# Kernel optimization log

Measured on AMD Instinct MI355X. Metric: run time of the kernel, lower is better.

The kernel has to match this reference:

```python
import jax, jax.numpy as jnp
import numpy as np

EMB, HID, NCH, CHK = 512, 1024, 16, 64   # hid_sz=1024, chunk_sz=64 -> 16 chunks
K, V = 5, 32000                           # n_mixtures, vocab
B, T = 8, 129
GATE = 4 * HID + 2 * NCH                  # i,f,o,g plus 2 master gates over chunks


def setup_inputs() -> dict:
    key = jax.random.key(0)
    ks = jax.random.split(key, 12)
    w = lambda k, shape: jax.random.normal(k, shape, jnp.float32) * 0.05
    return {
        "ys_token": jax.random.randint(ks[0], (B, T), 0, V),
        "emb": w(ks[1], (V, EMB)).at[0].set(0.0),  # padding_idx=0 row zeroed
        "Wx0": w(ks[2], (EMB, GATE)), "Wh0": w(ks[3], (HID, GATE)), "b0": jnp.zeros((GATE,), jnp.float32),
        "Wx1": w(ks[4], (HID, GATE)), "Wh1": w(ks[5], (HID, GATE)), "b1": jnp.zeros((GATE,), jnp.float32),
        "Wx2": w(ks[6], (HID, GATE)), "Wh2": w(ks[7], (HID, GATE)), "b2": jnp.zeros((GATE,), jnp.float32),
        "Wp": w(ks[8], (HID, K)), "bp": jnp.zeros((K,), jnp.float32),
        "Wl": w(ks[9], (HID, K * HID)), "bl": jnp.zeros((K * HID,), jnp.float32),
        "Wo": w(ks[10], (HID, V)), "bo": jnp.zeros((V,), jnp.float32),
    }


def _onlstm_cell(x, h, c, Wx, Wh, b):
    """One ON-LSTM step. Returns (h', c', master_forget_cumax)."""
    proj = x @ Wx + h @ Wh + b
    gates, masters = proj[:, : 4 * HID], proj[:, 4 * HID :]
    i, f, o, g = jnp.split(gates, 4, axis=-1)
    i, f, o = jax.nn.sigmoid(i), jax.nn.sigmoid(f), jax.nn.sigmoid(o)
    g = jnp.tanh(g)
    mf, mi = jnp.split(masters, 2, axis=-1)            # (B, NCH) each
    tf = jnp.cumsum(jax.nn.softmax(mf, -1), -1)        # master forget: cumax
    ti = 1.0 - jnp.cumsum(jax.nn.softmax(mi, -1), -1)  # master input: 1 - cumax
    tfe = jnp.repeat(tf, CHK, axis=-1)                 # expand chunks to HID
    tie = jnp.repeat(ti, CHK, axis=-1)
    w_ = tfe * tie
    c2 = (f * w_ + (tfe - w_)) * c + (i * w_ + (tie - w_)) * g
    h2 = o * jnp.tanh(c2)
    return h2, c2, tf


def reference(ys_token, emb, Wx0, Wh0, b0, Wx1, Wh1, b1, Wx2, Wh2, b2, Wp, bp, Wl, bl, Wo, bo):
    ys_in = ys_token[:, :-1]
    x = emb[ys_in]                                     # (B, T-1, EMB)
    z = jnp.zeros((B, HID), jnp.float32)

    def step(carry, xt):
        h0, c0, h1, c1, h2, c2 = carry
        h0, c0, _ = _onlstm_cell(xt, h0, c0, Wx0, Wh0, b0)
        h1, c1, tf1 = _onlstm_cell(h0, h1, c1, Wx1, Wh1, b1)  # s_layer = 1
        h2, c2, _ = _onlstm_cell(h1, h2, c2, Wx2, Wh2, b2)
        df = NCH - jnp.sum(tf1, -1)                    # expected split depth (B,)
        return (h0, c0, h1, c1, h2, c2), (h2, tf1, df)

    _, (outs, cf, df) = jax.lax.scan(step, (z, z, z, z, z, z), jnp.swapaxes(x, 0, 1))
    h = jnp.swapaxes(outs, 0, 1)                       # (B, L, HID)
    cf = jnp.swapaxes(cf, 0, 1)                        # (B, L, NCH)
    df = jnp.swapaxes(df, 0, 1)                        # (B, L)

    # Mixture-of-Softmaxes predictor
    log_prior = jax.nn.log_softmax(h @ Wp + bp, -1)    # (B, L, K)
    lat = jnp.tanh(h @ Wl + bl).reshape(B, T - 1, K, HID)
    mix = jax.nn.log_softmax(jnp.einsum("blkh,hv->blkv", lat, Wo) + bo, -1)
    logp = jax.nn.logsumexp(log_prior[..., None] + mix, axis=2)  # (B, L, V) log-probs

    gold = ys_token[:, 1:]
    mask = (gold != 0).astype(jnp.float32)
    nll = -jnp.take_along_axis(logp, gold[..., None], -1)[..., 0]
    per_seq = jnp.sum(nll * mask, 1) / (jnp.sum(mask, 1) + 1e-13)
    loss = jnp.mean(per_seq)
    pred = jnp.argmax(logp, -1)
    return loss, df, cf, pred
```

## Files before the change

kernel.cpp:

```cpp
#include <hip/hip_runtime.h>
#include <stdint.h>
#include <stddef.h>

#define TT   128
#define GATE 4128
#define VOC  32000
#define NWG  256

typedef float  f32x4 __attribute__((ext_vector_type(4)));
typedef short  bf16x8 __attribute__((ext_vector_type(8)));
typedef unsigned short u16x4 __attribute__((ext_vector_type(4)));

__device__ __forceinline__ float bf2f(ushort u){
  union { uint32_t i; float f; } c; c.i = ((uint32_t)u) << 16; return c.f;
}
__device__ __forceinline__ ushort f2bf(float x){
  uint32_t u = __builtin_bit_cast(uint32_t, x);
  uint32_t r = (u + 0x7fffu + ((u >> 16) & 1u)) >> 16;
  return (ushort)r;
}

__global__ void embed_kernel(const int* __restrict__ ys, const float* __restrict__ emb,
                             float* __restrict__ x){
  int r = blockIdx.x;
  int t = r >> 3, b = r & 7;
  int tok = ys[b*129 + t];
  f32x4 v = *(const f32x4*)&emb[(size_t)tok*512 + threadIdx.x*4];
  *(f32x4*)&x[(size_t)r*512 + threadIdx.x*4] = v;
}

__global__ void whT_kernel(const float* __restrict__ Wh, float* __restrict__ WhT){
  __shared__ float tile[32][33];
  int g0 = blockIdx.x*32, k0 = blockIdx.y*32;
  int tx = threadIdx.x, ty = threadIdx.y;
  for (int i = ty; i < 32; i += 8)
    tile[i][tx] = Wh[(size_t)(k0+i)*GATE + g0 + tx];
  __syncthreads();
  for (int i = ty; i < 32; i += 8)
    WhT[(size_t)(g0+i)*1024 + k0 + tx] = tile[tx][i];
}

__global__ void whmT_kernel(const float* __restrict__ Wh, float* __restrict__ WhmT){
  int idx = blockIdx.x*256 + threadIdx.x;
  int k = idx >> 5, c = idx & 31;
  WhmT[idx] = Wh[(size_t)k*GATE + 4096 + c];
}

template<int MODE>
__global__ __launch_bounds__(256) void gemm_f32_kernel(
    const float* __restrict__ X, const float* __restrict__ W, const float* __restrict__ bias,
    float* __restrict__ O1, int Kdim, int N)
{
  __shared__ float At[2][8][132];
  __shared__ float Bs[2][8][132];
  int tid = threadIdx.x;
  int n0 = blockIdx.x*128, r0 = blockIdx.y*128;
  int tx = tid & 15, ty = tid >> 4;
  int am = tid >> 1, akq = tid & 1;
  int bk = tid >> 5, bnc = tid & 31;
  float acc[8][8];
  #pragma unroll
  for (int i=0;i<8;i++)
    #pragma unroll
    for (int j=0;j<8;j++) acc[i][j]=0.f;
  {
    f32x4 av = *(const f32x4*)&X[(size_t)(r0+am)*Kdim + akq*4];
    At[0][akq*4+0][am]=av.x; At[0][akq*4+1][am]=av.y; At[0][akq*4+2][am]=av.z; At[0][akq*4+3][am]=av.w;
    int nb = n0 + bnc*4;
    f32x4 bv = {0.f,0.f,0.f,0.f};
    if (nb + 3 < N) bv = *(const f32x4*)&W[(size_t)bk*N + nb];
    *(f32x4*)&Bs[0][bk][bnc*4] = bv;
  }
  __syncthreads();
  int nk = Kdim >> 3;
  for (int ksb = 0; ksb < nk; ksb++){
    int cb = ksb & 1;
    if (ksb + 1 < nk){
      int k0 = (ksb+1)*8, bs = cb^1;
      f32x4 av = *(const f32x4*)&X[(size_t)(r0+am)*Kdim + k0 + akq*4];
      At[bs][akq*4+0][am]=av.x; At[bs][akq*4+1][am]=av.y; At[bs][akq*4+2][am]=av.z; At[bs][akq*4+3][am]=av.w;
      int nb = n0 + bnc*4;
      f32x4 bv = {0.f,0.f,0.f,0.f};
      if (nb + 3 < N) bv = *(const f32x4*)&W[(size_t)(k0+bk)*N + nb];
      *(f32x4*)&Bs[bs][bk][bnc*4] = bv;
    }
    #pragma unroll
    for (int k = 0; k < 8; k++){
      float a[8], b[8];
      *(f32x4*)&a[0] = *(const f32x4*)&At[cb][k][ty*8];
      *(f32x4*)&a[4] = *(const f32x4*)&At[cb][k][ty*8+4];
      *(f32x4*)&b[0] = *(const f32x4*)&Bs[cb][k][tx*8];
      *(f32x4*)&b[4] = *(const f32x4*)&Bs[cb][k][tx*8+4];
      #pragma unroll
      for (int i=0;i<8;i++)
        #pragma unroll
        for (int j=0;j<8;j++) acc[i][j] = fmaf(a[i], b[j], acc[i][j]);
    }
    __syncthreads();
  }
  #pragma unroll
  for (int i=0;i<8;i++){
    int r = r0 + ty*8 + i;
    #pragma unroll
    for (int j=0;j<8;j+=4){
      int n = n0 + tx*8 + j;
      if (n + 3 < N){
        f32x4 v;
        v.x = acc[i][j+0] + bias[n+0];
        v.y = acc[i][j+1] + bias[n+1];
        v.z = acc[i][j+2] + bias[n+2];
        v.w = acc[i][j+3] + bias[n+3];
        if (MODE == 1){
          v.x = tanhf(v.x); v.y = tanhf(v.y); v.z = tanhf(v.z); v.w = tanhf(v.w);
        }
        *(f32x4*)&O1[(size_t)r*N + n] = v;
      }
    }
  }
}

__global__ __launch_bounds__(256) void latsplit_kernel(const float* __restrict__ latf,
                                                       ushort* __restrict__ hi, ushort* __restrict__ lo){
  int i = (blockIdx.x*256 + threadIdx.x)*4;
  f32x4 v = *(const f32x4*)&latf[i];
  u16x4 h, l;
  #pragma unroll
  for (int j = 0; j < 4; j++){
    ushort hb = f2bf(v[j]);
    h[j] = hb;
    l[j] = f2bf(v[j] - bf2f(hb));
  }
  *(u16x4*)&hi[i] = h;
  *(u16x4*)&lo[i] = l;
}

__device__ __forceinline__ void gbar(int* flags, int* gen, int ep, int wg, int tid){
  if (wg == 0){
    if (tid == 0){
      __threadfence();
      __hip_atomic_store(&flags[0], ep, __ATOMIC_RELAXED, __HIP_MEMORY_SCOPE_AGENT);
    }
    if (tid < NWG){
      while (__hip_atomic_load(&flags[tid*16], __ATOMIC_RELAXED, __HIP_MEMORY_SCOPE_AGENT) < ep)
        __builtin_amdgcn_s_sleep(1);
    }
    __syncthreads();
    if (tid == 0){
      __threadfence();
      __hip_atomic_store(gen, ep, __ATOMIC_RELAXED, __HIP_MEMORY_SCOPE_AGENT);
      __threadfence();
    }
  } else {
    if (tid == 0){
      __threadfence();
      __hip_atomic_store(&flags[wg*16], ep, __ATOMIC_RELAXED, __HIP_MEMORY_SCOPE_AGENT);
      while (__hip_atomic_load(gen, __ATOMIC_RELAXED, __HIP_MEMORY_SCOPE_AGENT) < ep)
        __builtin_amdgcn_s_sleep(2);
      __threadfence();
    }
  }
}

__global__ __launch_bounds__(512) void scan_kernel(
    const float* __restrict__ A,
    const float* __restrict__ WhT,
    const float* __restrict__ WhmT,
    float* __restrict__ hbuf,
    float* __restrict__ H,
    float* __restrict__ cf_out, float* __restrict__ df_out,
    int* bar_flags, int* bar_gen, int* mflags, float* tfti)
{
  __shared__ __align__(16) float wls[1024*20];
  __shared__ __align__(16) float hls[1024*12];
  __shared__ __align__(16) float gpw[2][2][32][36];
  __shared__ float projg[8][16];
  __shared__ float cst[8][4];
  __shared__ float mpart[8][8][4];
  __shared__ float projmb[32];

  int tid = threadIdx.x, wg = blockIdx.x;
  int e0 = wg*4, chunk = wg >> 4;

  #pragma unroll
  for (int c = 0; c < 16; c++){
    int gcol = (c>>2)*1024 + e0 + (c&3);
    const float* src = WhT + (size_t)gcol*1024;
    for (int k = tid; k < 1024; k += 512)
      wls[k*20 + c] = src[k];
  }
  if (tid < 32) cst[tid & 7][tid >> 3] = 0.f;
  __syncthreads();

  int cq = tid >> 8;
  int bh = (tid >> 7) & 1;
  int kp = tid & 127;
  bool isM = (wg < 8);
  int mcg = tid & 7, mkp = tid >> 3;

  for (int t = 0; t < TT; t++){
    int rb = (t+1) & 1, wb = t & 1;
    float Ag = 0.f;
    if (tid < 128){
      int c = tid >> 3, b = tid & 7;
      Ag = A[(size_t)(t*8+b)*GATE + (c>>2)*1024 + e0 + (c&3)];
    }
    float Am = 0.f;
    if (isM && tid < 32) Am = A[(size_t)(t*8+wg)*GATE + 4096 + tid];

    {
      const f32x4* hb4 = (const f32x4*)&hbuf[rb*8192];
      #pragma unroll
      for (int s2 = 0; s2 < 4; s2++){
        int i4 = s2*512 + tid;
        f32x4 v = hb4[i4];
        int k = i4 >> 1, h2 = i4 & 1;
        *(f32x4*)&hls[k*12 + h2*4] = v;
      }
    }
    __syncthreads();

    if (isM){
      float macc[4] = {0.f,0.f,0.f,0.f};
      #pragma unroll
      for (int j = 0; j < 16; j++){
        int k = j*64 + mkp;
        f32x4 wm = *(const f32x4*)&WhmT[k*32 + mcg*4];
        float hv = hls[k*12 + wg];
        macc[0] += wm.x*hv; macc[1] += wm.y*hv; macc[2] += wm.z*hv; macc[3] += wm.w*hv;
      }
      #pragma unroll
      for (int off = 8; off < 64; off <<= 1){
        macc[0] += __shfl_xor(macc[0], off);
        macc[1] += __shfl_xor(macc[1], off);
        macc[2] += __shfl_xor(macc[2], off);
        macc[3] += __shfl_xor(macc[3], off);
      }
      if ((tid & 63) < 8){
        int wv = tid >> 6;
        mpart[wv][mcg][0] = macc[0]; mpart[wv][mcg][1] = macc[1];
        mpart[wv][mcg][2] = macc[2]; mpart[wv][mcg][3] = macc[3];
      }
      __syncthreads();
      if (tid < 32){
        float s = Am;
        #pragma unroll
        for (int wv = 0; wv < 8; wv++) s += mpart[wv][tid>>2][tid&3];
        projmb[tid] = s;
      }
      __syncthreads();
      if (tid == 0){
        float mx1 = -1e30f, mx2 = -1e30f;
        #pragma unroll
        for (int j = 0; j < 16; j++){
          mx1 = fmaxf(mx1, projmb[j]);
          mx2 = fmaxf(mx2, projmb[16+j]);
        }
        float e1[16], e2[16], s1 = 0.f, s2 = 0.f;
        #pragma unroll
        for (int j = 0; j < 16; j++){
          e1[j] = expf(projmb[j]    - mx1); s1 += e1[j];
          e2[j] = expf(projmb[16+j] - mx2); s2 += e2[j];
        }
        float r1 = 0.f, r2 = 0.f, tsum = 0.f;
        #pragma unroll
        for (int j = 0; j < 16; j++){
          r1 += e1[j]/s1; tfti[wg*16 + j] = r1; tsum += r1;
          r2 += e2[j]/s2; tfti[128 + wg*16 + j] = 1.f - r2;
        }
        if (cf_out != nullptr){
          #pragma unroll
          for (int j = 0; j < 16; j++) cf_out[(wg*TT + t)*16 + j] = tfti[wg*16 + j];
          df_out[wg*TT + t] = 16.0f - tsum;
        }
        __threadfence();
        __hip_atomic_store(&mflags[wg*16], t+1, __ATOMIC_RELAXED, __HIP_MEMORY_SCOPE_AGENT);
      }
    }

    float acc[8][4];
    #pragma unroll
    for (int c = 0; c < 8; c++)
      #pragma unroll
      for (int b2 = 0; b2 < 4; b2++) acc[c][b2] = 0.f;
    #pragma unroll
    for (int j = 0; j < 8; j++){
      int k = j*128 + kp;
      float wa[8], hb[4];
      *(f32x4*)&wa[0] = *(const f32x4*)&wls[k*20 + cq*8];
      *(f32x4*)&wa[4] = *(const f32x4*)&wls[k*20 + cq*8 + 4];
      *(f32x4*)&hb[0] = *(const f32x4*)&hls[k*12 + bh*4];
      #pragma unroll
      for (int c = 0; c < 8; c++)
        #pragma unroll
        for (int b2 = 0; b2 < 4; b2++)
          acc[c][b2] = fmaf(wa[c], hb[b2], acc[c][b2]);
    }
    #pragma unroll
    for (int c = 0; c < 8; c++)
      #pragma unroll
      for (int b2 = 0; b2 < 4; b2++){
        float v = acc[c][b2];
        v += __shfl_xor(v, 1);
        v += __shfl_xor(v, 2);
        acc[c][b2] = v;
      }
    if ((kp & 3) == 0){
      int kg = kp >> 2;
      #pragma unroll
      for (int c = 0; c < 8; c++){
        f32x4 v4 = { acc[c][0], acc[c][1], acc[c][2], acc[c][3] };
        *(f32x4*)&gpw[cq][bh][kg][c*4] = v4;
      }
    }
    __syncthreads();
    if (tid < 128){
      int c = tid >> 3, b = tid & 7;
      float s = Ag;
      #pragma unroll
      for (int g = 0; g < 32; g++) s += gpw[c>>3][b>>2][g][(c&7)*4 + (b&3)];
      projg[b][c] = s;
    }
    if (tid < 8){
      while (__hip_atomic_load(&mflags[tid*16], __ATOMIC_RELAXED, __HIP_MEMORY_SCOPE_AGENT) < t+1)
        __builtin_amdgcn_s_sleep(1);
    }
    __syncthreads();
    if (tid < 32){
      int b = tid & 7, e = tid >> 3;
      float gi = projg[b][e], gf = projg[b][4+e], go = projg[b][8+e], gg = projg[b][12+e];
      float iv = 1.f/(1.f+expf(-gi)), fv = 1.f/(1.f+expf(-gf)), ov = 1.f/(1.f+expf(-go));
      float gv = tanhf(gg);
      float tf = __hip_atomic_load(&tfti[b*16 + chunk],       __ATOMIC_RELAXED, __HIP_MEMORY_SCOPE_AGENT);
      float ti = __hip_atomic_load(&tfti[128 + b*16 + chunk], __ATOMIC_RELAXED, __HIP_MEMORY_SCOPE_AGENT);
      float w  = tf*ti;
      float c2 = (fv*w + (tf - w))*cst[b][e] + (iv*w + (ti - w))*gv;
      cst[b][e] = c2;
      float h2 = ov * tanhf(c2);
      hbuf[wb*8192 + (e0+e)*8 + b] = h2;
      H[(size_t)(t*8+b)*1024 + e0 + e] = h2;
    }
    __syncthreads();
    gbar(bar_flags, bar_gen, t+1, wg, tid);
    __syncthreads();
  }
}

__device__ __forceinline__ void stageA_lds(const ushort* gsrc, char* ldsbase, int row0, int k0, int tid){
  int lane = tid & 63, wv = tid >> 6;
  #pragma unroll
  for (int s = 0; s < 2; s++){
    int p = wv*1024 + s*4096 + lane*16;
    int row = p >> 6;
    int kg  = (p >> 4) & 3;
    int kgs = kg ^ ((row >> 1) & 3);
    const ushort* ga = gsrc + (size_t)(row0 + row)*1024 + k0 + kgs*8;
    __builtin_amdgcn_global_load_lds(
        (const __attribute__((address_space(1))) void*)ga,
        (__attribute__((address_space(3))) void*)(ldsbase + wv*1024 + s*4096),
        16, 0, 0);
  }
}
__device__ __forceinline__ void stageB(const float* __restrict__ Wo, int n0, int k0, int tid,
                                       char* bhi, char* blo){
  int kp = tid & 15, g = tid >> 4;
  const float* src = Wo + (size_t)(k0 + 2*kp)*VOC + n0 + g*8;
  f32x4 v00 = *(const f32x4*)(src);
  f32x4 v01 = *(const f32x4*)(src + 4);
  f32x4 v10 = *(const f32x4*)(src + VOC);
  f32x4 v11 = *(const f32x4*)(src + VOC + 4);
  int kg = kp >> 2, sub = kp & 3;
  #pragma unroll
  for (int j = 0; j < 8; j++){
    float x0 = (j < 4) ? v00[j] : v01[j-4];
    float x1 = (j < 4) ? v10[j] : v11[j-4];
    ushort h0 = f2bf(x0), h1 = f2bf(x1);
    ushort l0 = f2bf(x0 - bf2f(h0)), l1 = f2bf(x1 - bf2f(h1));
    int n = g*8 + j;
    int byte = n*64 + ((kg ^ ((n >> 1) & 3)) << 4) + sub*4;
    *(uint32_t*)(bhi + byte) = (uint32_t)h0 | ((uint32_t)h1 << 16);
    *(uint32_t*)(blo + byte) = (uint32_t)l0 | ((uint32_t)l1 << 16);
  }
}
__device__ __forceinline__ bf16x8 rdfrag(const char* base, int row, int kg){
  int byte = row*64 + ((kg ^ ((row >> 1) & 3)) << 4);
  return *(const bf16x8*)(base + byte);
}

__global__ __launch_bounds__(256) void wo_gemm_kernel(
    const ushort* __restrict__ Ahi, const ushort* __restrict__ Alo,
    const float* __restrict__ Wo, const float* __restrict__ bo,
    float* __restrict__ S, float* __restrict__ partials, int rowbase)
{
  __shared__ __align__(16) char smem[66560];
  __shared__ float bo_s[128];
  __shared__ float redm[128][2], reds[128][2];
  int tid = threadIdx.x;
  int nt = blockIdx.x, mt = blockIdx.y;
  int n0 = nt*128, row0loc = mt*128, row0 = rowbase + row0loc;
  if (tid < 128) bo_s[tid] = bo[n0 + tid];
  f32x4 acc[4][4] = {};

  stageA_lds(Ahi, smem + 0,    row0, 0, tid);
  stageA_lds(Alo, smem + 8192, row0, 0, tid);
  stageB(Wo, n0, 0, tid, smem + 16384, smem + 24576);
  __syncthreads();

  int lane = tid & 63, wv = tid >> 6;
  int wr = wv >> 1, wc = wv & 1;
  int rl = lane & 15, kgl = lane >> 4;
  for (int ks = 0; ks < 32; ks++){
    char* cb = smem + (ks & 1)*32768;
    if (ks + 1 < 32){
      char* nb2 = smem + ((ks+1) & 1)*32768;
      stageA_lds(Ahi, nb2,        row0, (ks+1)*32, tid);
      stageA_lds(Alo, nb2 + 8192, row0, (ks+1)*32, tid);
      stageB(Wo, n0, (ks+1)*32, tid, nb2 + 16384, nb2 + 24576);
    }
    bf16x8 ah[4], al[4], bh[4], bl2[4];
    #pragma unroll
    for (int m = 0; m < 4; m++){
      int row = wr*64 + m*16 + rl;
      ah[m] = rdfrag(cb,        row, kgl);
      al[m] = rdfrag(cb + 8192, row, kgl);
    }
    #pragma unroll
    for (int n = 0; n < 4; n++){
      int rw = wc*64 + n*16 + rl;
      bh[n]  = rdfrag(cb + 16384, rw, kgl);
      bl2[n] = rdfrag(cb + 24576, rw, kgl);
    }
    #pragma unroll
    for (int m = 0; m < 4; m++)
      #pragma unroll
      for (int n = 0; n < 4; n++){
        acc[m][n] = __builtin_amdgcn_mfma_f32_16x16x32_bf16(ah[m], bh[n],  acc[m][n], 0,0,0);
        acc[m][n] = __builtin_amdgcn_mfma_f32_16x16x32_bf16(ah[m], bl2[n], acc[m][n], 0,0,0);
        acc[m][n] = __builtin_amdgcn_mfma_f32_16x16x32_bf16(al[m], bh[n],  acc[m][n], 0,0,0);
      }
    __syncthreads();
  }

  float* st = (float*)smem;
  #pragma unroll
  for (int m = 0; m < 4; m++){
    int rb = wr*64 + m*16 + (lane >> 4)*4;
    #pragma unroll
    for (int n = 0; n < 4; n++){
      int col = wc*64 + n*16 + rl;
      #pragma unroll
      for (int j = 0; j < 4; j++)
        st[(rb + j)*130 + col] = acc[m][n][j];
    }
  }
  __syncthreads();
  int row = tid >> 1, half = tid & 1;
  float lmax = -1e30f;
  for (int jc = 0; jc < 64; jc += 4){
    f32x4 v;
    #pragma unroll
    for (int j = 0; j < 4; j++){
      float x = st[row*130 + half*64 + jc + j] + bo_s[half*64 + jc + j];
      st[row*130 + half*64 + jc + j] = x;
      v[j] = x;
      lmax = fmaxf(lmax, x);
    }
    *(f32x4*)&S[(size_t)(row0loc + row)*VOC + n0 + half*64 + jc] = v;
  }
  redm[row][half] = lmax;
  __syncthreads();
  float rm = fmaxf(redm[row][0], redm[row][1]);
  float lsum = 0.f;
  for (int jc = 0; jc < 64; jc++)
    lsum += expf(st[row*130 + half*64 + jc] - rm);
  reds[row][half] = lsum;
  __syncthreads();
  if (half == 0){
    float2 pr; pr.x = rm; pr.y = reds[row][0] + reds[row][1];
    *(float2*)&partials[((size_t)(row0loc + row)*250 + nt)*2] = pr;
  }
}

__global__ void zfin_kernel(const float* __restrict__ partials, double* __restrict__ Zc, int CH){
  int rl = blockIdx.x*256 + threadIdx.x;
  if (rl >= CH) return;
  float m = -1e30f;
  for (int t2 = 0; t2 < 250; t2++) m = fmaxf(m, partials[((size_t)rl*250 + t2)*2]);
  double s = 0.0;
  for (int t2 = 0; t2 < 250; t2++){
    float pm = partials[((size_t)rl*250 + t2)*2];
    float se = partials[((size_t)rl*250 + t2)*2 + 1];
    s += exp((double)pm - (double)m)*(double)se;
  }
  Zc[rl] = (double)m + log(s);
}

__device__ __forceinline__ float cand_q(const float* __restrict__ srow, int v,
                                        float l0, float l1, float l2, float l3, float l4){
  float t0 = l0 + srow[v];
  float t1 = l1 + srow[VOC   + v];
  float t2 = l2 + srow[2*VOC + v];
  float t3 = l3 + srow[3*VOC + v];
  float t4 = l4 + srow[4*VOC + v];
  float m = fmaxf(fmaxf(fmaxf(t0,t1),fmaxf(t2,t3)),t4);
  return m + logf(expf(t0-m)+expf(t1-m)+expf(t2-m)+expf(t3-m)+expf(t4-m));
}
__global__ __launch_bounds__(256) void cand_kernel(
    const float* __restrict__ S, const double* __restrict__ lp, const double* __restrict__ Z,
    int* __restrict__ cand, int rbase)
{
  int g = blockIdx.x; int r = rbase + g; int tid = threadIdx.x;
  __shared__ float lpk[5];
  __shared__ float rq[256]; __shared__ int rv[256];
  __shared__ int cnt; __shared__ int list[64];
  if (tid < 5) lpk[tid] = (float)(lp[r*5 + tid] - Z[r*5 + tid]);
  if (tid == 0) cnt = 0;
  __syncthreads();
  float l0 = lpk[0], l1 = lpk[1], l2 = lpk[2], l3 = lpk[3], l4 = lpk[4];
  const float* srow = S + (size_t)(g*5)*VOC;
  float bq = -1e30f; int bv = 0;
  for (int v = tid; v < VOC; v += 256){
    float q = cand_q(srow, v, l0,l1,l2,l3,l4);
    if (q > bq){ bq = q; bv = v; }
  }
  rq[tid] = bq; rv[tid] = bv; __syncthreads();
  for (int s = 128; s > 0; s >>= 1){
    if (tid < s){
      if (rq[tid+s] > rq[tid] || (rq[tid+s] == rq[tid] && rv[tid+s] < rv[tid])){
        rq[tid] = rq[tid+s]; rv[tid] = rv[tid+s];
      }
    }
    __syncthreads();
  }
  float M = rq[0]; int argv = rv[0];
  for (int v = tid; v < VOC; v += 256){
    float q = cand_q(srow, v, l0,l1,l2,l3,l4);
    if (q >= M - 0.02f && v != argv){
      int ix = atomicAdd(&cnt, 1);
      if (ix < 63) list[ix] = v;
    }
  }
  __syncthreads();
  int nc = cnt < 63 ? cnt : 63;
  if (tid == 0){ cand[r*66] = nc + 1; cand[r*66 + 1] = argv; }
  if (tid < nc) cand[r*66 + 2 + tid] = list[tid];
}

__global__ __launch_bounds__(256) void refine_kernel(
    const float* __restrict__ lat, const float* __restrict__ Wo, const float* __restrict__ bo,
    const double* __restrict__ lp, const double* __restrict__ Z,
    const int* __restrict__ cand, const int* __restrict__ ys,
    float* __restrict__ nll, float* __restrict__ pred_out)
{
  int r = blockIdx.x, tid = threadIdx.x;
  int b = r & 7, l = r >> 3;
  int nc = cand[r*66];
  if (nc < 0) nc = 0;
  if (nc > 64) nc = 64;
  __shared__ double dred[5][4];
  __shared__ double bestval; __shared__ int bestv;
  if (tid == 0){ bestval = -1e300; bestv = 0; }
  __syncthreads();
  int gold = ys[b*129 + l + 1];
  for (int ci = 0; ci <= nc; ci++){
    int v = (ci < nc) ? cand[r*66 + 1 + ci] : gold;
    double p0=0,p1=0,p2=0,p3=0,p4=0;
    for (int h = tid; h < 1024; h += 256){
      double w = (double)Wo[(size_t)h*VOC + v];
      p0 += (double)lat[((size_t)r*5+0)*1024 + h]*w;
      p1 += (double)lat[((size_t)r*5+1)*1024 + h]*w;
      p2 += (double)lat[((size_t)r*5+2)*1024 + h]*w;
      p3 += (double)lat[((size_t)r*5+3)*1024 + h]*w;
      p4 += (double)lat[((size_t)r*5+4)*1024 + h]*w;
    }
    #pragma unroll
    for (int off = 32; off; off >>= 1){
      p0 += __shfl_down(p0, off); p1 += __shfl_down(p1, off);
      p2 += __shfl_down(p2, off); p3 += __shfl_down(p3, off);
      p4 += __shfl_down(p4, off);
    }
    if ((tid & 63) == 0){
      int w = tid >> 6;
      dred[0][w]=p0; dred[1][w]=p1; dred[2][w]=p2; dred[3][w]=p3; dred[4][w]=p4;
    }
    __syncthreads();
    if (tid == 0){
      double bv = (double)bo[v];
      double tk[5]; double mx = -1e300;
      #pragma unroll
      for (int k = 0; k < 5; k++){
        double sk = dred[k][0]+dred[k][1]+dred[k][2]+dred[k][3] + bv;
        tk[k] = (lp[r*5+k] - Z[r*5+k]) + sk;
        mx = tk[k] > mx ? tk[k] : mx;
      }
      double q = mx + log(exp(tk[0]-mx)+exp(tk[1]-mx)+exp(tk[2]-mx)+exp(tk[3]-mx)+exp(tk[4]-mx));
      if (ci < nc){
        if (q > bestval || (q == bestval && v < bestv)){ bestval = q; bestv = v; }
      } else {
        nll[r] = (float)(-q);
      }
    }
    __syncthreads();
  }
  if (tid == 0) pred_out[b*TT + l] = (float)bestv;
}

__global__ __launch_bounds__(64) void prior_kernel(
    const float* __restrict__ H2, const float* __restrict__ Wp, const float* __restrict__ bp,
    double* __restrict__ lp)
{
  int r = blockIdx.x, tid = threadIdx.x;
  double p0=0,p1=0,p2=0,p3=0,p4=0;
  for (int h = tid; h < 1024; h += 64){
    double x = (double)H2[(size_t)r*1024 + h];
    const float* w = &Wp[h*5];
    p0 += x*(double)w[0]; p1 += x*(double)w[1]; p2 += x*(double)w[2];
    p3 += x*(double)w[3]; p4 += x*(double)w[4];
  }
  #pragma unroll
  for (int off = 32; off; off >>= 1){
    p0 += __shfl_down(p0, off); p1 += __shfl_down(p1, off);
    p2 += __shfl_down(p2, off); p3 += __shfl_down(p3, off);
    p4 += __shfl_down(p4, off);
  }
  if (tid == 0){
    double lg[5] = { p0+(double)bp[0], p1+(double)bp[1], p2+(double)bp[2], p3+(double)bp[3], p4+(double)bp[4] };
    double mx = lg[0];
    #pragma unroll
    for (int k = 1; k < 5; k++) mx = lg[k] > mx ? lg[k] : mx;
    double s = 0;
    #pragma unroll
    for (int k = 0; k < 5; k++) s += exp(lg[k]-mx);
    double lse = mx + log(s);
    #pragma unroll
    for (int k = 0; k < 5; k++) lp[r*5+k] = lg[k] - lse;
  }
}

__global__ void loss_kernel(const float* __restrict__ nll, const int* __restrict__ ys,
                            float* __restrict__ out){
  int tid = threadIdx.x;
  __shared__ float ps[8];
  if (tid < 8){
    float s = 0.f, ms = 0.f;
    for (int l = 0; l < TT; l++){
      int gold = ys[tid*129 + l + 1];
      float m = (gold != 0) ? 1.f : 0.f;
      s  += nll[l*8 + tid]*m;
      ms += m;
    }
    ps[tid] = s/(ms + 1e-13f);
  }
  __syncthreads();
  if (tid == 0){
    float t = 0.f;
    for (int b = 0; b < 8; b++) t += ps[b];
    out[0] = t/8.f;
  }
}

extern "C" void kernel_launch(void* const* d_in, const int* in_sizes, int n_in,
                              void* d_out, int out_size, void* d_ws, size_t ws_size,
                              hipStream_t stream)
{
  (void)in_sizes; (void)n_in; (void)out_size;
  const int*   ys  = (const int*)  d_in[0];
  const float* emb = (const float*)d_in[1];
  const float* Wx0 = (const float*)d_in[2];
  const float* Wh0 = (const float*)d_in[3];
  const float* b0  = (const float*)d_in[4];
  const float* Wx1 = (const float*)d_in[5];
  const float* Wh1 = (const float*)d_in[6];
  const float* b1  = (const float*)d_in[7];
  const float* Wx2 = (const float*)d_in[8];
  const float* Wh2 = (const float*)d_in[9];
  const float* b2  = (const float*)d_in[10];
  const float* Wp  = (const float*)d_in[11];
  const float* bp  = (const float*)d_in[12];
  const float* Wl  = (const float*)d_in[13];
  const float* bl  = (const float*)d_in[14];
  const float* Wo  = (const float*)d_in[15];
  const float* bo  = (const float*)d_in[16];
  float* out = (float*)d_out;

  char* ws = (char*)d_ws;
  size_t off = 0;
  auto alloc = [&](size_t bytes){ size_t o = off; off += (bytes + 255) & ~(size_t)255; return o; };
  size_t o_hbuf = alloc(2*8192*4);
  size_t o_bars = alloc(3*(NWG*16 + 16)*sizeof(int));
  size_t o_mfl  = alloc(3*8*16*sizeof(int));
  size_t zero_bytes = off;
  size_t o_tfti = alloc(256*4);
  size_t o_x    = alloc((size_t)1024*512*4);
  size_t o_whT  = alloc((size_t)GATE*1024*4);
  size_t o_whmT = alloc((size_t)1024*32*4);
  size_t o_A    = alloc((size_t)1024*GATE*4);
  size_t o_H0   = alloc((size_t)1024*1024*4);
  size_t o_H1   = alloc((size_t)1024*1024*4);
  size_t o_H2   = alloc((size_t)1024*1024*4);
  size_t o_lp   = alloc((size_t)1024*5*8);
  size_t o_latf = alloc((size_t)1024*5120*4);
  size_t o_lath = alloc((size_t)5120*1024*2);
  size_t o_latl = alloc((size_t)5120*1024*2);
  size_t o_Z    = alloc((size_t)5120*8);
  size_t o_cand = alloc((size_t)1024*66*4);
  size_t o_nll  = alloc((size_t)1024*4);
  int CH = 1280;
  if (off + (size_t)CH*250*2*4 + (size_t)CH*VOC*4 > ws_size) CH = 640;
  size_t o_part = alloc((size_t)CH*250*2*4);
  size_t o_s    = alloc((size_t)CH*VOC*4);
  (void)o_s;

  float*  hbuf  = (float*) (ws + o_hbuf);
  int*    bars  = (int*)   (ws + o_bars);
  int*    mfl   = (int*)   (ws + o_mfl);
  float*  tfti  = (float*) (ws + o_tfti);
  float*  xbuf  = (float*) (ws + o_x);
  float*  whT   = (float*) (ws + o_whT);
  float*  whmT  = (float*) (ws + o_whmT);
  float*  Abuf  = (float*) (ws + o_A);
  float*  H0    = (float*) (ws + o_H0);
  float*  H1    = (float*) (ws + o_H1);
  float*  H2    = (float*) (ws + o_H2);
  double* lpbuf = (double*)(ws + o_lp);
  float*  latf  = (float*) (ws + o_latf);
  ushort* lath  = (ushort*)(ws + o_lath);
  ushort* latl  = (ushort*)(ws + o_latl);
  double* Zbuf  = (double*)(ws + o_Z);
  int*    candb = (int*)   (ws + o_cand);
  float*  nllb  = (float*) (ws + o_nll);
  float*  partb = (float*) (ws + o_part);
  float*  Sbuf  = (float*) (ws + o_s);

  int perl = NWG*16 + 16;
  int* flags0 = bars;             int* gen0 = flags0 + NWG*16;
  int* flags1 = bars + perl;      int* gen1 = flags1 + NWG*16;
  int* flags2 = bars + 2*perl;    int* gen2 = flags2 + NWG*16;
  int* mfl0 = mfl;  int* mfl1 = mfl + 8*16;  int* mfl2 = mfl + 16*16;

  hipMemsetAsync(d_ws, 0, zero_bytes, stream);
  embed_kernel<<<1024, 128, 0, stream>>>(ys, emb, xbuf);

  gemm_f32_kernel<0><<<dim3(33,8), 256, 0, stream>>>(xbuf, Wx0, b0, Abuf, 512, GATE);
  whT_kernel<<<dim3(129,32), dim3(32,8), 0, stream>>>(Wh0, whT);
  whmT_kernel<<<128, 256, 0, stream>>>(Wh0, whmT);
  scan_kernel<<<NWG, 512, 0, stream>>>(Abuf, whT, whmT, hbuf, H0, nullptr, nullptr,
                                       flags0, gen0, mfl0, tfti);
  gemm_f32_kernel<0><<<dim3(33,8), 256, 0, stream>>>(H0, Wx1, b1, Abuf, 1024, GATE);
  whT_kernel<<<dim3(129,32), dim3(32,8), 0, stream>>>(Wh1, whT);
  whmT_kernel<<<128, 256, 0, stream>>>(Wh1, whmT);
  hipMemsetAsync(hbuf, 0, 2*8192*4, stream);
  scan_kernel<<<NWG, 512, 0, stream>>>(Abuf, whT, whmT, hbuf, H1, out + 1025, out + 1,
                                       flags1, gen1, mfl1, tfti);
  gemm_f32_kernel<0><<<dim3(33,8), 256, 0, stream>>>(H1, Wx2, b2, Abuf, 1024, GATE);
  whT_kernel<<<dim3(129,32), dim3(32,8), 0, stream>>>(Wh2, whT);
  whmT_kernel<<<128, 256, 0, stream>>>(Wh2, whmT);
  hipMemsetAsync(hbuf, 0, 2*8192*4, stream);
  scan_kernel<<<NWG, 512, 0, stream>>>(Abuf, whT, whmT, hbuf, H2, nullptr, nullptr,
                                       flags2, gen2, mfl2, tfti);

  prior_kernel<<<1024, 64, 0, stream>>>(H2, Wp, bp, lpbuf);
  gemm_f32_kernel<1><<<dim3(40,8), 256, 0, stream>>>(H2, Wl, bl, latf, 1024, 5120);
  latsplit_kernel<<<5120, 256, 0, stream>>>(latf, lath, latl);

  int nchunks = 5120 / CH;
  for (int c = 0; c < nchunks; c++){
    wo_gemm_kernel<<<dim3(250, CH/128), 256, 0, stream>>>(lath, latl, Wo, bo, Sbuf, partb, c*CH);
    zfin_kernel<<<(CH + 255)/256, 256, 0, stream>>>(partb, Zbuf + c*CH, CH);
    cand_kernel<<<CH/5, 256, 0, stream>>>(Sbuf, lpbuf, Zbuf, candb, c*(CH/5));
  }
  refine_kernel<<<1024, 256, 0, stream>>>(latf, Wo, bo, lpbuf, Zbuf, candb, ys, nllb, out + 17409);
  loss_kernel<<<1, 64, 0, stream>>>(nllb, ys, out);
}
```

Baseline: 10.26 ms.

## Pre-split Wo into swizzled bf16 hi/lo images and fuse lat split into GEMM

```diff
diff --git a/kernel.cpp b/kernel.cpp
--- a/kernel.cpp
+++ b/kernel.cpp
@@ -46,10 +46,34 @@
   WhmT[idx] = Wh[(size_t)k*GATE + 4096 + c];
 }
 
+__global__ __launch_bounds__(256) void wosplit_kernel(const float* __restrict__ Wo,
+                                                      uint32_t* __restrict__ hi_img,
+                                                      uint32_t* __restrict__ lo_img){
+  __shared__ float tile[32][132];
+  int ks = blockIdx.x, nt = blockIdx.y;
+  int tid = threadIdx.x;
+  for (int i = tid; i < 4096; i += 256)
+    tile[i>>7][i&127] = Wo[(size_t)(ks*32 + (i>>7))*VOC + nt*128 + (i&127)];
+  __syncthreads();
+  size_t base = ((size_t)(nt*32 + ks)) << 11;
+  for (int i = tid; i < 2048; i += 256){
+    int p = i*4;
+    int row = p >> 6, kgpos = (p >> 4) & 3, sub = (p >> 2) & 3;
+    int kg = kgpos ^ ((row >> 1) & 3);
+    int ke = kg*8 + 2*sub;
+    float x0 = tile[ke][row], x1 = tile[ke+1][row];
+    ushort h0 = f2bf(x0), h1 = f2bf(x1);
+    ushort l0 = f2bf(x0 - bf2f(h0)), l1 = f2bf(x1 - bf2f(h1));
+    hi_img[base + i] = (uint32_t)h0 | ((uint32_t)h1 << 16);
+    lo_img[base + i] = (uint32_t)l0 | ((uint32_t)l1 << 16);
+  }
+}
+
 template<int MODE>
 __global__ __launch_bounds__(256) void gemm_f32_kernel(
     const float* __restrict__ X, const float* __restrict__ W, const float* __restrict__ bias,
-    float* __restrict__ O1, int Kdim, int N)
+    float* __restrict__ O1, ushort* __restrict__ O2, ushort* __restrict__ O3,
+    int Kdim, int N)
 {
   __shared__ float At[2][8][132];
   __shared__ float Bs[2][8][132];
@@ -110,28 +134,24 @@
         v.y = acc[i][j+1] + bias[n+1];
         v.z = acc[i][j+2] + bias[n+2];
         v.w = acc[i][j+3] + bias[n+3];
-        if (MODE == 1){
+        if (MODE >= 1){
           v.x = tanhf(v.x); v.y = tanhf(v.y); v.z = tanhf(v.z); v.w = tanhf(v.w);
         }
         *(f32x4*)&O1[(size_t)r*N + n] = v;
-      }
-    }
-  }
-}
-
-__global__ __launch_bounds__(256) void latsplit_kernel(const float* __restrict__ latf,
-                                                       ushort* __restrict__ hi, ushort* __restrict__ lo){
-  int i = (blockIdx.x*256 + threadIdx.x)*4;
-  f32x4 v = *(const f32x4*)&latf[i];
-  u16x4 h, l;
-  #pragma unroll
-  for (int j = 0; j < 4; j++){
-    ushort hb = f2bf(v[j]);
-    h[j] = hb;
-    l[j] = f2bf(v[j] - bf2f(hb));
-  }
-  *(u16x4*)&hi[i] = h;
-  *(u16x4*)&lo[i] = l;
+        if (MODE == 2){
+          u16x4 h, l;
+          #pragma unroll
+          for (int q = 0; q < 4; q++){
+            ushort hb = f2bf(v[q]);
+            h[q] = hb;
+            l[q] = f2bf(v[q] - bf2f(hb));
+          }
+          *(u16x4*)&O2[(size_t)r*N + n] = h;
+          *(u16x4*)&O3[(size_t)r*N + n] = l;
+        }
+      }
+    }
+  }
 }
 
 __device__ __forceinline__ void gbar(int* flags, int* gen, int ep, int wg, int tid){
@@ -248,30 +268,35 @@
         projmb[tid] = s;
       }
       __syncthreads();
+      if (tid < 32){
+        int half = tid >> 4, j = tid & 15;
+        float x = projmb[tid];
+        float mx = x;
+        #pragma unroll
+        for (int o = 1; o < 16; o <<= 1) mx = fmaxf(mx, __shfl_xor(mx, o));
+        float e = expf(x - mx);
+        float ssum = e;
+        #pragma unroll
+        for (int o = 1; o < 16; o <<= 1) ssum += __shfl_xor(ssum, o);
+        float sm = e / ssum;
+        float c = sm;
+        #pragma unroll
+        for (int o = 1; o < 16; o <<= 1){
+          float t2 = __shfl_up(c, o);
+          if (j >= o) c += t2;
+        }
+        float outv = half ? (1.f - c) : c;
+        tfti[half*128 + wg*16 + j] = outv;
+        if (cf_out != nullptr && half == 0){
+          cf_out[(wg*TT + t)*16 + j] = c;
+          float ts = c;
+          #pragma unroll
+          for (int o = 1; o < 16; o <<= 1) ts += __shfl_xor(ts, o);
+          if (j == 0) df_out[wg*TT + t] = 16.f - ts;
+        }
+      }
+      __syncthreads();
       if (tid == 0){
-        float mx1 = -1e30f, mx2 = -1e30f;
-        #pragma unroll
-        for (int j = 0; j < 16; j++){
-          mx1 = fmaxf(mx1, projmb[j]);
-          mx2 = fmaxf(mx2, projmb[16+j]);
-        }
-        float e1[16], e2[16], s1 = 0.f, s2 = 0.f;
-        #pragma unroll
-        for (int j = 0; j < 16; j++){
-          e1[j] = expf(projmb[j]    - mx1); s1 += e1[j];
-          e2[j] = expf(projmb[16+j] - mx2); s2 += e2[j];
-        }
-        float r1 = 0.f, r2 = 0.f, tsum = 0.f;
-        #pragma unroll
-        for (int j = 0; j < 16; j++){
-          r1 += e1[j]/s1; tfti[wg*16 + j] = r1; tsum += r1;
-          r2 += e2[j]/s2; tfti[128 + wg*16 + j] = 1.f - r2;
-        }
-        if (cf_out != nullptr){
-          #pragma unroll
-          for (int j = 0; j < 16; j++) cf_out[(wg*TT + t)*16 + j] = tfti[wg*16 + j];
-          df_out[wg*TT + t] = 16.0f - tsum;
-        }
         __threadfence();
         __hip_atomic_store(&mflags[wg*16], t+1, __ATOMIC_RELAXED, __HIP_MEMORY_SCOPE_AGENT);
       }
@@ -360,8 +385,20 @@
         16, 0, 0);
   }
 }
-__device__ __forceinline__ void stageB(const float* __restrict__ Wo, int n0, int k0, int tid,
-                                       char* bhi, char* blo){
+__device__ __forceinline__ void stageB_pre(const char* img, char* lds, int nt, int ks, int tid){
+  int lane = tid & 63, wv = tid >> 6;
+  const char* base = img + (((size_t)(nt*32 + ks)) << 13);
+  #pragma unroll
+  for (int s = 0; s < 2; s++){
+    int p = wv*1024 + s*4096 + lane*16;
+    __builtin_amdgcn_global_load_lds(
+        (const __attribute__((address_space(1))) void*)(base + p),
+        (__attribute__((address_space(3))) void*)(lds + p),
+        16, 0, 0);
+  }
+}
+__device__ __forceinline__ void stageB_cv(const float* __restrict__ Wo, int n0, int k0, int tid,
+                                          char* bhi, char* blo){
   int kp = tid & 15, g = tid >> 4;
   const float* src = Wo + (size_t)(k0 + 2*kp)*VOC + n0 + g*8;
   f32x4 v00 = *(const f32x4*)(src);
@@ -386,9 +423,11 @@
   return *(const bf16x8*)(base + byte);
 }
 
+template<int PRE>
 __global__ __launch_bounds__(256) void wo_gemm_kernel(
     const ushort* __restrict__ Ahi, const ushort* __restrict__ Alo,
     const float* __restrict__ Wo, const float* __restrict__ bo,
+    const char* __restrict__ wohi_img, const char* __restrict__ wolo_img,
     float* __restrict__ S, float* __restrict__ partials, int rowbase)
 {
   __shared__ __align__(16) char smem[66560];
@@ -402,7 +441,12 @@
 
   stageA_lds(Ahi, smem + 0,    row0, 0, tid);
   stageA_lds(Alo, smem + 8192, row0, 0, tid);
-  stageB(Wo, n0, 0, tid, smem + 16384, smem + 24576);
+  if (PRE){
+    stageB_pre(wohi_img, smem + 16384, nt, 0, tid);
+    stageB_pre(wolo_img, smem + 24576, nt, 0, tid);
+  } else {
+    stageB_cv(Wo, n0, 0, tid, smem + 16384, smem + 24576);
+  }
   __syncthreads();
 
   int lane = tid & 63, wv = tid >> 6;
@@ -414,7 +458,12 @@
       char* nb2 = smem + ((ks+1) & 1)*32768;
       stageA_lds(Ahi, nb2,        row0, (ks+1)*32, tid);
       stageA_lds(Alo, nb2 + 8192, row0, (ks+1)*32, tid);
-      stageB(Wo, n0, (ks+1)*32, tid, nb2 + 16384, nb2 + 24576);
+      if (PRE){
+        stageB_pre(wohi_img, nb2 + 16384, nt, ks+1, tid);
+        stageB_pre(wolo_img, nb2 + 24576, nt, ks+1, tid);
+      } else {
+        stageB_cv(Wo, n0, (ks+1)*32, tid, nb2 + 16384, nb2 + 24576);
+      }
     }
     bf16x8 ah[4], al[4], bh[4], bl2[4];
     #pragma unroll
@@ -704,8 +753,21 @@
   size_t o_Z    = alloc((size_t)5120*8);
   size_t o_cand = alloc((size_t)1024*66*4);
   size_t o_nll  = alloc((size_t)1024*4);
-  int CH = 1280;
-  if (off + (size_t)CH*250*2*4 + (size_t)CH*VOC*4 > ws_size) CH = 640;
+  size_t base   = off;
+
+  const size_t woimg = (size_t)250*32*8192;
+  auto need = [&](int ch, int pre){
+    return base + (pre ? 2*((woimg + 255) & ~(size_t)255) : 0)
+                + (((size_t)ch*250*2*4 + 255) & ~(size_t)255)
+                + (((size_t)ch*VOC*4 + 255) & ~(size_t)255);
+  };
+  int PRE, CH;
+  if      (need(1280,1) <= ws_size){ PRE=1; CH=1280; }
+  else if (need(640, 1) <= ws_size){ PRE=1; CH=640;  }
+  else if (need(1280,0) <= ws_size){ PRE=0; CH=1280; }
+  else                              { PRE=0; CH=640;  }
+  size_t o_wohi = 0, o_wolo = 0;
+  if (PRE){ o_wohi = alloc(woimg); o_wolo = alloc(woimg); }
   size_t o_part = alloc((size_t)CH*250*2*4);
   size_t o_s    = alloc((size_t)CH*VOC*4);
   (void)o_s;
@@ -728,6 +790,8 @@
   double* Zbuf  = (double*)(ws + o_Z);
   int*    candb = (int*)   (ws + o_cand);
   float*  nllb  = (float*) (ws + o_nll);
+  char*   wohi  = ws + o_wohi;
+  char*   wolo  = ws + o_wolo;
   float*  partb = (float*) (ws + o_part);
   float*  Sbuf  = (float*) (ws + o_s);
 
@@ -739,19 +803,21 @@
 
   hipMemsetAsync(d_ws, 0, zero_bytes, stream);
   embed_kernel<<<1024, 128, 0, stream>>>(ys, emb, xbuf);
-
-  gemm_f32_kernel<0><<<dim3(33,8), 256, 0, stream>>>(xbuf, Wx0, b0, Abuf, 512, GATE);
+  if (PRE)
+    wosplit_kernel<<<dim3(32,250), 256, 0, stream>>>(Wo, (uint32_t*)wohi, (uint32_t*)wolo);
+
+  gemm_f32_kernel<0><<<dim3(33,8), 256, 0, stream>>>(xbuf, Wx0, b0, Abuf, nullptr, nullptr, 512, GATE);
   whT_kernel<<<dim3(129,32), dim3(32,8), 0, stream>>>(Wh0, whT);
   whmT_kernel<<<128, 256, 0, stream>>>(Wh0, whmT);
   scan_kernel<<<NWG, 512, 0, stream>>>(Abuf, whT, whmT, hbuf, H0, nullptr, nullptr,
                                        flags0, gen0, mfl0, tfti);
-  gemm_f32_kernel<0><<<dim3(33,8), 256, 0, stream>>>(H0, Wx1, b1, Abuf, 1024, GATE);
+  gemm_f32_kernel<0><<<dim3(33,8), 256, 0, stream>>>(H0, Wx1, b1, Abuf, nullptr, nullptr, 1024, GATE);
   whT_kernel<<<dim3(129,32), dim3(32,8), 0, stream>>>(Wh1, whT);
   whmT_kernel<<<128, 256, 0, stream>>>(Wh1, whmT);
   hipMemsetAsync(hbuf, 0, 2*8192*4, stream);
   scan_kernel<<<NWG, 512, 0, stream>>>(Abuf, whT, whmT, hbuf, H1, out + 1025, out + 1,
                                        flags1, gen1, mfl1, tfti);
-  gemm_f32_kernel<0><<<dim3(33,8), 256, 0, stream>>>(H1, Wx2, b2, Abuf, 1024, GATE);
+  gemm_f32_kernel<0><<<dim3(33,8), 256, 0, stream>>>(H1, Wx2, b2, Abuf, nullptr, nullptr, 1024, GATE);
   whT_kernel<<<dim3(129,32), dim3(32,8), 0, stream>>>(Wh2, whT);
   whmT_kernel<<<128, 256, 0, stream>>>(Wh2, whmT);
   hipMemsetAsync(hbuf, 0, 2*8192*4, stream);
@@ -759,12 +825,14 @@
                                        flags2, gen2, mfl2, tfti);
 
   prior_kernel<<<1024, 64, 0, stream>>>(H2, Wp, bp, lpbuf);
-  gemm_f32_kernel<1><<<dim3(40,8), 256, 0, stream>>>(H2, Wl, bl, latf, 1024, 5120);
-  latsplit_kernel<<<5120, 256, 0, stream>>>(latf, lath, latl);
+  gemm_f32_kernel<2><<<dim3(40,8), 256, 0, stream>>>(H2, Wl, bl, latf, lath, latl, 1024, 5120);
 
   int nchunks = 5120 / CH;
   for (int c = 0; c < nchunks; c++){
-    wo_gemm_kernel<<<dim3(250, CH/128), 256, 0, stream>>>(lath, latl, Wo, bo, Sbuf, partb, c*CH);
+    if (PRE)
+      wo_gemm_kernel<1><<<dim3(250, CH/128), 256, 0, stream>>>(lath, latl, Wo, bo, wohi, wolo, Sbuf, partb, c*CH);
+    else
+      wo_gemm_kernel<0><<<dim3(250, CH/128), 256, 0, stream>>>(lath, latl, Wo, bo, nullptr, nullptr, Sbuf, partb, c*CH);
     zfin_kernel<<<(CH + 255)/256, 256, 0, stream>>>(partb, Zbuf + c*CH, CH);
     cand_kernel<<<CH/5, 256, 0, stream>>>(Sbuf, lpbuf, Zbuf, candb, c*(CH/5));
   }
```

New measurement: 9.598 ms. 6.5% less time.
